# Kernel optimization log

Measured on AMD Instinct MI355X. Metric: run time of the kernel, lower is better.

## Reference

```python
import jax, jax.numpy as jnp
import numpy as np

TOPK = 13
NUM_CLASSES = 80
ALPHA = 1.0
BETA = 6.0
EPS = 1e-09
BS, NA, M = 8, 33600, 64
IMG = 1280.0


def setup_inputs() -> dict:
    key = jax.random.key(0)
    k = jax.random.split(key, 8)
    pd_scores = jax.random.uniform(k[0], (BS, NA, NUM_CLASSES), jnp.float32)
    pd_xy = jax.random.uniform(k[1], (BS, NA, 2), jnp.float32) * IMG
    pd_r = jax.random.uniform(k[2], (BS, NA, 1), jnp.float32) * 63.0 + 1.0
    pd_circles = jnp.concatenate([pd_xy, pd_r], axis=-1)
    anc_points = jax.random.uniform(k[3], (NA, 2), jnp.float32) * IMG
    gt_labels = jax.random.randint(k[4], (BS, M, 1), 0, NUM_CLASSES)
    gt_xy = jax.random.uniform(k[5], (BS, M, 2), jnp.float32) * IMG
    gt_r = jax.random.uniform(k[6], (BS, M, 1), jnp.float32) * 120.0 + 8.0
    gt_circles = jnp.concatenate([gt_xy, gt_r], axis=-1)
    mask_gt = (jax.random.uniform(k[7], (BS, M, 1)) > 0.2).astype(jnp.float32)
    return {"pd_scores": pd_scores, "pd_circles": pd_circles, "anc_points": anc_points,
            "gt_labels": gt_labels, "gt_circles": gt_circles, "mask_gt": mask_gt}


def _circle_iou(gt_circles, pd_circles):
    # gt_circles: (bs, M, 3); pd_circles: (bs, NA, 3) -> iou (bs, M, NA)
    c0 = gt_circles[:, :, None, :2]          # (bs, M, 1, 2)
    r0 = gt_circles[:, :, None, 2]           # (bs, M, 1)
    c1 = pd_circles[:, None, :, :2]          # (bs, 1, NA, 2)
    r1 = pd_circles[:, None, :, 2]           # (bs, 1, NA)
    d = jnp.sqrt(jnp.sum((c0 - c1) ** 2, axis=-1) + 1e-12)  # (bs, M, NA)
    # lens (partial-overlap) area, numerically safe
    d1 = (r0 ** 2 - r1 ** 2 + d ** 2) / (2.0 * d)
    d2 = d - d1
    a0 = r0 ** 2 * jnp.arccos(jnp.clip(d1 / jnp.maximum(r0, EPS), -1.0, 1.0)) \
         - d1 * jnp.sqrt(jnp.clip(r0 ** 2 - d1 ** 2, 0.0, None))
    a1 = r1 ** 2 * jnp.arccos(jnp.clip(d2 / jnp.maximum(r1, EPS), -1.0, 1.0)) \
         - d2 * jnp.sqrt(jnp.clip(r1 ** 2 - d2 ** 2, 0.0, None))
    lens = a0 + a1
    contained = jnp.pi * jnp.minimum(r0, r1) ** 2
    inter = jnp.where(d >= r0 + r1, 0.0, jnp.where(d <= jnp.abs(r0 - r1), contained, lens))
    area0 = jnp.pi * r0 ** 2
    area1 = jnp.pi * r1 ** 2
    union = area0 + area1 - inter
    return jnp.where(union > 0, inter / union, 0.0)


def _assigner(pd_scores, pd_circles, anc_points, gt_labels, gt_circles, mask_gt):
    bs, na, nc = pd_scores.shape
    m = gt_circles.shape[1]
    mask_gt_f = mask_gt[..., 0]  # (bs, m)

    # select_candidates_in_gts: anchor point inside gt circle
    d_anc = jnp.sqrt(jnp.sum((anc_points[None, None, :, :] - gt_circles[:, :, None, :2]) ** 2, axis=-1))
    mask_in_gts = (d_anc < gt_circles[:, :, None, 2]).astype(pd_scores.dtype)  # (bs, m, na)
    mask_valid = mask_in_gts * mask_gt_f[:, :, None]

    # get_box_metrics: gather class scores at gt label, circle IoU, align metric
    gl = jnp.clip(gt_labels[..., 0], 0, nc - 1)  # (bs, m) int
    ps_t = jnp.transpose(pd_scores, (0, 2, 1))   # (bs, nc, na)
    bbox_scores = jnp.take_along_axis(ps_t, jnp.broadcast_to(gl[:, :, None], (bs, m, na)), axis=1)
    bbox_scores = bbox_scores * mask_valid
    overlaps = _circle_iou(gt_circles, pd_circles) * mask_valid  # (bs, m, na)
    align_metric = (bbox_scores ** ALPHA) * (overlaps ** BETA)

    # select_topk_candidates
    topk_metrics, topk_idxs = jax.lax.top_k(align_metric, TOPK)   # (bs, m, topk)
    topk_mask = jnp.broadcast_to(mask_gt_f[:, :, None] > 0, topk_idxs.shape)
    topk_idxs = jnp.where(topk_mask, topk_idxs, 0)
    counts = jnp.zeros((bs, m, na), pd_scores.dtype).at[
        jnp.arange(bs)[:, None, None], jnp.arange(m)[None, :, None], topk_idxs].add(1.0)
    mask_topk = jnp.where(counts > 1, 0.0, counts)
    mask_pos = mask_topk * mask_in_gts * mask_gt_f[:, :, None]

    # select_highest_overlaps: resolve anchors assigned to multiple gts
    fg = jnp.sum(mask_pos, axis=1)                       # (bs, na)
    multi = (fg[:, None, :] > 1)                          # (bs, 1->m, na)
    max_idx = jnp.argmax(overlaps, axis=1)                # (bs, na)
    is_max = jax.nn.one_hot(max_idx, m, axis=1, dtype=mask_pos.dtype)  # (bs, m, na)
    mask_pos = jnp.where(multi, is_max, mask_pos)
    fg_mask = jnp.sum(mask_pos, axis=1)                   # (bs, na)
    target_gt_idx = jnp.argmax(mask_pos, axis=1)          # (bs, na)

    # get_targets
    bidx = jnp.arange(bs)[:, None]
    target_labels = jnp.clip(gt_labels[..., 0][bidx, target_gt_idx], 0, None)   # (bs, na)
    target_circles = gt_circles[bidx, target_gt_idx]                             # (bs, na, 3)
    target_scores = jax.nn.one_hot(target_labels, nc, dtype=pd_scores.dtype)
    target_scores = jnp.where(fg_mask[..., None] > 0, target_scores, 0.0)

    # normalize scores by aligned metric
    am = align_metric * mask_pos
    pos_align = jnp.max(am, axis=-1, keepdims=True)                # (bs, m, 1)
    pos_overlaps = jnp.max(overlaps * mask_pos, axis=-1, keepdims=True)
    norm = jnp.max(am * pos_overlaps / (pos_align + EPS), axis=1)[..., None]  # (bs, na, 1)
    target_scores = target_scores * norm
    return target_labels, target_circles, target_scores, fg_mask > 0, target_gt_idx


def reference(pd_scores, pd_circles, anc_points, gt_labels, gt_circles, mask_gt):
    return _assigner(pd_scores, pd_circles, anc_points, gt_labels, gt_circles, mask_gt)
```

## Files before the change

### kernel.cpp

```cpp
#include <hip/hip_runtime.h>
#include <math.h>

#define B   8
#define NA  33600
#define M   64
#define NC  80
#define KK  13
#define EPSF 1e-9f
#define PIF 3.14159265358979323846f

#define NPOS 1536
#define NBM  (B * M)
#define SPB  (M * KK)


__device__ __forceinline__ float circle_iou(float gx, float gy, float gr,
                                            float px, float py, float pr) {
    float dx = gx - px, dy = gy - py;
    float d  = sqrtf(dx * dx + dy * dy + 1e-12f);
    float r0sq = gr * gr, r1sq = pr * pr;
    float d1 = (r0sq - r1sq + d * d) / (2.0f * d);
    float d2 = d - d1;
    float t0 = fminf(fmaxf(d1 / fmaxf(gr, EPSF), -1.0f), 1.0f);
    float t1 = fminf(fmaxf(d2 / fmaxf(pr, EPSF), -1.0f), 1.0f);
    float a0 = r0sq * acosf(t0) - d1 * sqrtf(fmaxf(r0sq - d1 * d1, 0.0f));
    float a1 = r1sq * acosf(t1) - d2 * sqrtf(fmaxf(r1sq - d2 * d2, 0.0f));
    float lens = a0 + a1;
    float rmin = fminf(gr, pr);
    float contained = PIF * rmin * rmin;
    float inter = (d >= gr + pr) ? 0.0f
                : ((d <= fabsf(gr - pr)) ? contained : lens);
    float uni = PIF * r0sq + PIF * r1sq - inter;
    return (uni > 0.0f) ? inter / uni : 0.0f;
}


__global__ __launch_bounds__(1024)
void k_discover(const float* __restrict__ pd_scores, const float* __restrict__ pd_circles,
                const float* __restrict__ anc, const int* __restrict__ gt_labels,
                const float* __restrict__ gt_circles, const float* __restrict__ mask_gt,
                int* __restrict__ wlist, int* __restrict__ assigned,
                float* __restrict__ am_val) {
    int bm = blockIdx.x;
    int b  = bm / M;
    int tid = threadIdx.x;

    const int SL = (B * NA) / NBM;
    int s0 = bm * SL;
    if (tid < SL) { assigned[s0 + tid] = -1; am_val[s0 + tid] = 0.0f; }

    __shared__ int   s_pcnt;
    __shared__ int   s_pa[NPOS];
    __shared__ float s_pv[NPOS];
    __shared__ int   s_win[KK];

    float gmask = mask_gt[bm];
    if (!(gmask > 0.0f)) {
        if (tid < KK) wlist[bm * KK + tid] = -1;
        return;
    }

    float gx = gt_circles[bm * 3 + 0];
    float gy = gt_circles[bm * 3 + 1];
    float gr = gt_circles[bm * 3 + 2];
    int gl = gt_labels[bm];
    gl = gl < 0 ? 0 : (gl > NC - 1 ? NC - 1 : gl);

    if (tid == 0) s_pcnt = 0;
    __syncthreads();

    const float2* pdc2 = reinterpret_cast<const float2*>(pd_circles + (size_t)b * NA * 3);
    for (int q = tid; q < NA / 2; q += 1024) {
        float4 ap = reinterpret_cast<const float4*>(anc)[q];
        float2 p0 = pdc2[3 * q + 0];
        float2 p1 = pdc2[3 * q + 1];
        float2 p2 = pdc2[3 * q + 2];
        {
            float dx = ap.x - gx, dy = ap.y - gy;
            if (sqrtf(dx * dx + dy * dy) < gr) {
                float px = p0.x, py = p0.y, pr = p1.x;
                float cdx = gx - px, cdy = gy - py;
                float dc = sqrtf(cdx * cdx + cdy * cdy + 1e-12f);
                if (dc < gr + pr) {
                    float ov = circle_iou(gx, gy, gr, px, py, pr);
                    if (ov > 0.0f) {
                        float sc = pd_scores[((size_t)b * NA + 2 * q) * NC + gl];
                        float o2 = ov * ov;
                        float met = sc * (o2 * o2 * o2);
                        if (met > 0.0f) {
                            int p = atomicAdd(&s_pcnt, 1);
                            if (p < NPOS) { s_pa[p] = 2 * q; s_pv[p] = met; }
                        }
                    }
                }
            }
        }
        {
            float dx = ap.z - gx, dy = ap.w - gy;
            if (sqrtf(dx * dx + dy * dy) < gr) {
                float px = p1.y, py = p2.x, pr = p2.y;
                float cdx = gx - px, cdy = gy - py;
                float dc = sqrtf(cdx * cdx + cdy * cdy + 1e-12f);
                if (dc < gr + pr) {
                    float ov = circle_iou(gx, gy, gr, px, py, pr);
                    if (ov > 0.0f) {
                        float sc = pd_scores[((size_t)b * NA + 2 * q + 1) * NC + gl];
                        float o2 = ov * ov;
                        float met = sc * (o2 * o2 * o2);
                        if (met > 0.0f) {
                            int p = atomicAdd(&s_pcnt, 1);
                            if (p < NPOS) { s_pa[p] = 2 * q + 1; s_pv[p] = met; }
                        }
                    }
                }
            }
        }
    }
    __syncthreads();
    int pcnt = s_pcnt; if (pcnt > NPOS) pcnt = NPOS;

    if (tid >= 64) return;

    for (int k = 0; k < KK; k++) {
        float bv = 0.0f; int ba = 0x7fffffff; int bp = -1;
        for (int i = tid; i < pcnt; i += 64) {
            float v = s_pv[i];
            if (v > 0.0f) {
                int a = s_pa[i];
                if (v > bv || (v == bv && a < ba)) { bv = v; ba = a; bp = i; }
            }
        }
        for (int off = 32; off > 0; off >>= 1) {
            float v2 = __shfl_xor(bv, off);
            int   a2 = __shfl_xor(ba, off);
            int   p2 = __shfl_xor(bp, off);
            if (v2 > bv || (v2 == bv && a2 < ba)) { bv = v2; ba = a2; bp = p2; }
        }
        if (tid == 0) {
            if (bp >= 0) { s_win[k] = ba; s_pv[bp] = -1.0f; }
            else s_win[k] = -2;
        }
    }

    int defmask = 0;
    for (int k = 0; k < KK; k++) if (s_win[k] == -2) defmask |= (1 << k);
    if (defmask) {
        int base = 0;
        while (defmask && base < NA) {
            int idx = base + tid;
            bool freez = (idx < NA);
            for (int i = 0; i < pcnt; i++)
                freez = freez && (s_pa[i] != idx);
            unsigned long long msk = __ballot(freez);
            while (msk && defmask) {
                int bit = __ffsll((long long)msk) - 1; msk &= msk - 1;
                int k2  = __ffs(defmask) - 1;          defmask &= defmask - 1;
                if (tid == 0) s_win[k2] = base + bit;
            }
            base += 64;
        }
        while (defmask) {
            int k2 = __ffs(defmask) - 1; defmask &= defmask - 1;
            if (tid == 0) s_win[k2] = -1;
        }
    }

    if (tid < KK) {
        int a = s_win[tid];
        int outv = -1;
        if (a >= 0) {
            float ax = anc[2 * a], ay = anc[2 * a + 1];
            float dx = ax - gx, dy = ay - gy;
            if (sqrtf(dx * dx + dy * dy) < gr) outv = a;
        }
        wlist[bm * KK + tid] = outv;
    }
}


__global__ __launch_bounds__(1024)
void k_resolve(const float* __restrict__ pd_scores, const float* __restrict__ pd_circles,
               const float* __restrict__ anc, const int* __restrict__ gt_labels,
               const float* __restrict__ gt_circles, const float* __restrict__ mask_gt,
               const int* __restrict__ wlist,
               int* __restrict__ assigned, float* __restrict__ am_val,
               int* __restrict__ pos_align_i, int* __restrict__ pos_ov_i) {
    int b = blockIdx.x;
    int tid = threadIdx.x;

    __shared__ unsigned int s_cnt[NA / 4 + 1];
    __shared__ float s_gx[M], s_gy[M], s_gr[M];
    __shared__ int   s_gl[M], s_act[M];
    __shared__ int   s_posa[M], s_poso[M];
    __shared__ int   s_multi[512];
    __shared__ int   s_nm;

    if (tid < M) {
        int gi = b * M + tid;
        s_act[tid] = mask_gt[gi] > 0.0f;
        s_gx[tid] = gt_circles[gi * 3 + 0];
        s_gy[tid] = gt_circles[gi * 3 + 1];
        s_gr[tid] = gt_circles[gi * 3 + 2];
        int l = gt_labels[gi];
        s_gl[tid] = l < 0 ? 0 : (l > NC - 1 ? NC - 1 : l);
        s_posa[tid] = 0; s_poso[tid] = 0;
    }
    if (tid == 0) s_nm = 0;
    for (int w = tid; w < NA / 4 + 1; w += 1024) s_cnt[w] = 0;
    __syncthreads();

    int a = -1, m = -1; unsigned int prev = 0;
    if (tid < SPB) {
        a = wlist[b * SPB + tid];
        m = tid / KK;
        if (a >= 0) {
            unsigned int sh = 8u * (a & 3);
            unsigned int old = atomicAdd(&s_cnt[a >> 2], 1u << sh);
            prev = (old >> sh) & 0xFFu;
        }
    }
    __syncthreads();

    bool single = false;
    if (a >= 0) {
        unsigned int c = (s_cnt[a >> 2] >> (8u * (a & 3))) & 0xFFu;
        if (c == 1u) single = true;
        else if (prev == 0u) { int i2 = atomicAdd(&s_nm, 1); s_multi[i2] = a; }
    }
    if (single) {
        int i = b * NA + a;
        float gx = s_gx[m], gy = s_gy[m], gr = s_gr[m];
        float px = pd_circles[(size_t)i * 3 + 0];
        float py = pd_circles[(size_t)i * 3 + 1];
        float pr = pd_circles[(size_t)i * 3 + 2];
        float cdx = gx - px, cdy = gy - py;
        float dc = sqrtf(cdx * cdx + cdy * cdy + 1e-12f);
        float ov = (dc >= gr + pr) ? 0.0f : circle_iou(gx, gy, gr, px, py, pr);
        float met = 0.0f;
        if (ov > 0.0f) {
            float sc = pd_scores[(size_t)i * NC + s_gl[m]];
            float o2 = ov * ov;
            met = sc * (o2 * o2 * o2);
        }
        assigned[i] = m;
        am_val[i]   = met;
        atomicMax(&s_posa[m], __float_as_int(met));
        atomicMax(&s_poso[m], __float_as_int(ov));
    }
    __syncthreads();

    int lane = tid & 63, w = tid >> 6;
    int nm = s_nm;
    for (int r = w; r < nm; r += 16) {
        int am_ = s_multi[r];
        int i = b * NA + am_;
        float ax = anc[2 * am_], ay = anc[2 * am_ + 1];
        float px = pd_circles[(size_t)i * 3 + 0];
        float py = pd_circles[(size_t)i * 3 + 1];
        float pr = pd_circles[(size_t)i * 3 + 2];
        float ov = 0.0f;
        if (s_act[lane]) {
            float gx = s_gx[lane], gy = s_gy[lane], gr = s_gr[lane];
            float dx = ax - gx, dy = ay - gy;
            if (sqrtf(dx * dx + dy * dy) < gr) {
                float cdx = gx - px, cdy = gy - py;
                float dc = sqrtf(cdx * cdx + cdy * cdy + 1e-12f);
                ov = (dc >= gr + pr) ? 0.0f : circle_iou(gx, gy, gr, px, py, pr);
            }
        }
        float bv = ov; int bmx = lane;
        for (int off = 32; off > 0; off >>= 1) {
            float v2 = __shfl_xor(bv, off);
            int   m2 = __shfl_xor(bmx, off);
            if (v2 > bv || (v2 == bv && m2 < bmx)) { bv = v2; bmx = m2; }
        }
        if (lane == 0) {
            float met = 0.0f;
            if (bv > 0.0f) {
                float sc = pd_scores[(size_t)i * NC + s_gl[bmx]];
                float o2 = bv * bv;
                met = sc * (o2 * o2 * o2);
            }
            assigned[i] = bmx;
            am_val[i]   = met;
            atomicMax(&s_posa[bmx], __float_as_int(met));
            atomicMax(&s_poso[bmx], __float_as_int(bv));
        }
    }
    __syncthreads();

    if (tid < M) {
        pos_align_i[b * M + tid] = s_posa[tid];
        pos_ov_i[b * M + tid]    = s_poso[tid];
    }
}


__global__ void k_out(const int* __restrict__ assigned, const float* __restrict__ am_val,
                      const int* __restrict__ pos_align_i, const int* __restrict__ pos_ov_i,
                      const int* __restrict__ gt_labels, const float* __restrict__ gt_circles,
                      float* __restrict__ out_labels, float* __restrict__ out_circ,
                      float* __restrict__ out_scores, float* __restrict__ out_fg,
                      float* __restrict__ out_gtidx) {
    const int QPR = NC / 4;
    int q = blockIdx.x * blockDim.x + threadIdx.x;
    if (q >= B * NA * QPR) return;
    int row = q / QPR;
    int c0  = (q - row * QPR) * 4;
    int b   = row / NA;

    int g = assigned[row];
    int gidx = 0; float fg = 0.0f; float norm = 0.0f;
    if (g >= 0) {
        gidx = g; fg = 1.0f;
        float pa = __int_as_float(pos_align_i[b * M + g]);
        float po = __int_as_float(pos_ov_i[b * M + g]);
        norm = am_val[row] * po / (pa + EPSF);
    }
    int rawl = gt_labels[b * M + gidx];
    int lbl = rawl < 0 ? 0 : rawl;

    float4 v = make_float4(0.f, 0.f, 0.f, 0.f);
    if (g >= 0) {
        int off = lbl - c0;
        if (off >= 0 && off < 4) ((float*)&v)[off] = norm;
    }
    reinterpret_cast<float4*>(out_scores)[q] = v;

    if (c0 == 0) {
        out_labels[row] = (float)lbl;
        out_circ[(size_t)row * 3 + 0] = gt_circles[(b * M + gidx) * 3 + 0];
        out_circ[(size_t)row * 3 + 1] = gt_circles[(b * M + gidx) * 3 + 1];
        out_circ[(size_t)row * 3 + 2] = gt_circles[(b * M + gidx) * 3 + 2];
        out_fg[row]    = fg;
        out_gtidx[row] = (float)gidx;
    }
}


extern "C" void kernel_launch(void* const* d_in, const int* in_sizes, int n_in,
                              void* d_out, int out_size, void* d_ws, size_t ws_size,
                              hipStream_t stream) {
    const float* pd_scores  = (const float*)d_in[0];
    const float* pd_circles = (const float*)d_in[1];
    const float* anc        = (const float*)d_in[2];
    const int*   gt_labels  = (const int*)  d_in[3];
    const float* gt_circles = (const float*)d_in[4];
    const float* mask_gt    = (const float*)d_in[5];

    char* w = (char*)d_ws;
    int*   wlist       = (int*)w;   w += (size_t)NBM * KK * sizeof(int);
    int*   assigned    = (int*)w;   w += (size_t)B * NA * sizeof(int);
    float* am_val      = (float*)w; w += (size_t)B * NA * sizeof(float);
    int*   pos_align_i = (int*)w;   w += (size_t)B * M * sizeof(int);
    int*   pos_ov_i    = (int*)w;   w += (size_t)B * M * sizeof(int);

    float* out        = (float*)d_out;
    float* out_labels = out;
    float* out_circ   = out_labels + (size_t)B * NA;
    float* out_scores = out_circ + (size_t)B * NA * 3;
    float* out_fg     = out_scores + (size_t)B * NA * NC;
    float* out_gtidx  = out_fg + (size_t)B * NA;

    k_discover<<<NBM, 1024, 0, stream>>>(pd_scores, pd_circles, anc, gt_labels,
                                         gt_circles, mask_gt,
                                         wlist, assigned, am_val);

    k_resolve<<<B, 1024, 0, stream>>>(pd_scores, pd_circles, anc, gt_labels,
                                      gt_circles, mask_gt, wlist,
                                      assigned, am_val, pos_align_i, pos_ov_i);

    int nq = B * NA * (NC / 4);
    k_out<<<(nq + 255) / 256, 256, 0, stream>>>(assigned, am_val,
                                                pos_align_i, pos_ov_i,
                                                gt_labels, gt_circles,
                                                out_labels, out_circ, out_scores,
                                                out_fg, out_gtidx);
}
```

Before: 83.19 us.

## Invert discovery loop to anchor-major chunks and move top-k into resolve kernel

The per-(batch,gt) discovery kernel, which streamed all 33600 anchors once for every gt, is replaced by an anchor-chunk kernel. Each thread loads one anchor's prediction once and tests it against all 64 gts held in shared memory, writing compacted (anchor,gt,metric) candidates to per-chunk regions. The resolve kernel then gathers these candidates into a shared pool, runs per-gt top-k selection with one wave per gt, and reuses the stored metric instead of recomputing it. This removes 64x redundant anchor reads, but top-k now runs in only 8 blocks, and the fixed candidate capacities (96 per chunk, 96 per gt) can silently drop candidates.

```diff
diff --git a/kernel.cpp b/kernel.cpp
--- a/kernel.cpp
+++ b/kernel.cpp
@@ -9,9 +9,12 @@
 #define EPSF 1e-9f
 #define PIF 3.14159265358979323846f
 
-#define NPOS 1536
-#define NBM  (B * M)
-#define SPB  (M * KK)
+#define CHK   256
+#define NCHK  132
+#define BCAP  96
+#define REG   (1 + 2 * BCAP)
+#define FCAP  4096
+#define GCAP  96
 
 
 __device__ __forceinline__ float circle_iou(float gx, float gy, float gr,
@@ -35,165 +38,98 @@
 }
 
 
+__global__ __launch_bounds__(CHK)
+void k_build(const float* __restrict__ pd_scores, const float* __restrict__ pd_circles,
+             const float* __restrict__ anc, const int* __restrict__ gt_labels,
+             const float* __restrict__ gt_circles, const float* __restrict__ mask_gt,
+             int* __restrict__ breg, int* __restrict__ assigned,
+             float* __restrict__ am_val) {
+    int chunk = blockIdx.x;
+    int b     = blockIdx.y;
+    int tid   = threadIdx.x;
+
+    __shared__ float s_gx[M], s_gy[M], s_gr[M];
+    __shared__ int   s_gl[M], s_act[M];
+    __shared__ int   s_cnt;
+    __shared__ int   s_pk[BCAP];
+    __shared__ int   s_mv[BCAP];
+
+    if (tid < M) {
+        int gi = b * M + tid;
+        s_act[tid] = mask_gt[gi] > 0.0f;
+        s_gx[tid] = gt_circles[gi * 3 + 0];
+        s_gy[tid] = gt_circles[gi * 3 + 1];
+        s_gr[tid] = gt_circles[gi * 3 + 2];
+        int l = gt_labels[gi];
+        s_gl[tid] = l < 0 ? 0 : (l > NC - 1 ? NC - 1 : l);
+    }
+    if (tid == 0) s_cnt = 0;
+    __syncthreads();
+
+    int a = chunk * CHK + tid;
+    if (a < NA) {
+        int i = b * NA + a;
+        assigned[i] = -1;
+        am_val[i]   = 0.0f;
+        float2 ap = reinterpret_cast<const float2*>(anc)[a];
+        float px = pd_circles[(size_t)i * 3 + 0];
+        float py = pd_circles[(size_t)i * 3 + 1];
+        float pr = pd_circles[(size_t)i * 3 + 2];
+
+        for (int m = 0; m < M; m++) {
+            if (!s_act[m]) continue;
+            float gx = s_gx[m], gy = s_gy[m], gr = s_gr[m];
+            float dxa = ap.x - gx, dya = ap.y - gy;
+            if (!(sqrtf(dxa * dxa + dya * dya) < gr)) continue;
+            float cdx = gx - px, cdy = gy - py;
+            float dc = sqrtf(cdx * cdx + cdy * cdy + 1e-12f);
+            if (dc >= gr + pr) continue;
+            float ov = circle_iou(gx, gy, gr, px, py, pr);
+            if (!(ov > 0.0f)) continue;
+            float sc = pd_scores[(size_t)i * NC + s_gl[m]];
+            float o2 = ov * ov;
+            float met = sc * (o2 * o2 * o2);
+            if (met > 0.0f) {
+                int p = atomicAdd(&s_cnt, 1);
+                if (p < BCAP) { s_pk[p] = (a << 6) | m; s_mv[p] = __float_as_int(met); }
+            }
+        }
+    }
+    __syncthreads();
+
+    int cnt = s_cnt; if (cnt > BCAP) cnt = BCAP;
+    int rbase = (b * NCHK + chunk) * REG;
+    if (tid == 0) breg[rbase] = cnt;
+    if (tid < cnt) {
+        breg[rbase + 1 + tid]        = s_pk[tid];
+        breg[rbase + 1 + BCAP + tid] = s_mv[tid];
+    }
+}
+
+
 __global__ __launch_bounds__(1024)
-void k_discover(const float* __restrict__ pd_scores, const float* __restrict__ pd_circles,
-                const float* __restrict__ anc, const int* __restrict__ gt_labels,
-                const float* __restrict__ gt_circles, const float* __restrict__ mask_gt,
-                int* __restrict__ wlist, int* __restrict__ assigned,
-                float* __restrict__ am_val) {
-    int bm = blockIdx.x;
-    int b  = bm / M;
-    int tid = threadIdx.x;
-
-    const int SL = (B * NA) / NBM;
-    int s0 = bm * SL;
-    if (tid < SL) { assigned[s0 + tid] = -1; am_val[s0 + tid] = 0.0f; }
-
-    __shared__ int   s_pcnt;
-    __shared__ int   s_pa[NPOS];
-    __shared__ float s_pv[NPOS];
-    __shared__ int   s_win[KK];
-
-    float gmask = mask_gt[bm];
-    if (!(gmask > 0.0f)) {
-        if (tid < KK) wlist[bm * KK + tid] = -1;
-        return;
-    }
-
-    float gx = gt_circles[bm * 3 + 0];
-    float gy = gt_circles[bm * 3 + 1];
-    float gr = gt_circles[bm * 3 + 2];
-    int gl = gt_labels[bm];
-    gl = gl < 0 ? 0 : (gl > NC - 1 ? NC - 1 : gl);
-
-    if (tid == 0) s_pcnt = 0;
-    __syncthreads();
-
-    const float2* pdc2 = reinterpret_cast<const float2*>(pd_circles + (size_t)b * NA * 3);
-    for (int q = tid; q < NA / 2; q += 1024) {
-        float4 ap = reinterpret_cast<const float4*>(anc)[q];
-        float2 p0 = pdc2[3 * q + 0];
-        float2 p1 = pdc2[3 * q + 1];
-        float2 p2 = pdc2[3 * q + 2];
-        {
-            float dx = ap.x - gx, dy = ap.y - gy;
-            if (sqrtf(dx * dx + dy * dy) < gr) {
-                float px = p0.x, py = p0.y, pr = p1.x;
-                float cdx = gx - px, cdy = gy - py;
-                float dc = sqrtf(cdx * cdx + cdy * cdy + 1e-12f);
-                if (dc < gr + pr) {
-                    float ov = circle_iou(gx, gy, gr, px, py, pr);
-                    if (ov > 0.0f) {
-                        float sc = pd_scores[((size_t)b * NA + 2 * q) * NC + gl];
-                        float o2 = ov * ov;
-                        float met = sc * (o2 * o2 * o2);
-                        if (met > 0.0f) {
-                            int p = atomicAdd(&s_pcnt, 1);
-                            if (p < NPOS) { s_pa[p] = 2 * q; s_pv[p] = met; }
-                        }
-                    }
-                }
-            }
-        }
-        {
-            float dx = ap.z - gx, dy = ap.w - gy;
-            if (sqrtf(dx * dx + dy * dy) < gr) {
-                float px = p1.y, py = p2.x, pr = p2.y;
-                float cdx = gx - px, cdy = gy - py;
-                float dc = sqrtf(cdx * cdx + cdy * cdy + 1e-12f);
-                if (dc < gr + pr) {
-                    float ov = circle_iou(gx, gy, gr, px, py, pr);
-                    if (ov > 0.0f) {
-                        float sc = pd_scores[((size_t)b * NA + 2 * q + 1) * NC + gl];
-                        float o2 = ov * ov;
-                        float met = sc * (o2 * o2 * o2);
-                        if (met > 0.0f) {
-                            int p = atomicAdd(&s_pcnt, 1);
-                            if (p < NPOS) { s_pa[p] = 2 * q + 1; s_pv[p] = met; }
-                        }
-                    }
-                }
-            }
-        }
-    }
-    __syncthreads();
-    int pcnt = s_pcnt; if (pcnt > NPOS) pcnt = NPOS;
-
-    if (tid >= 64) return;
-
-    for (int k = 0; k < KK; k++) {
-        float bv = 0.0f; int ba = 0x7fffffff; int bp = -1;
-        for (int i = tid; i < pcnt; i += 64) {
-            float v = s_pv[i];
-            if (v > 0.0f) {
-                int a = s_pa[i];
-                if (v > bv || (v == bv && a < ba)) { bv = v; ba = a; bp = i; }
-            }
-        }
-        for (int off = 32; off > 0; off >>= 1) {
-            float v2 = __shfl_xor(bv, off);
-            int   a2 = __shfl_xor(ba, off);
-            int   p2 = __shfl_xor(bp, off);
-            if (v2 > bv || (v2 == bv && a2 < ba)) { bv = v2; ba = a2; bp = p2; }
-        }
-        if (tid == 0) {
-            if (bp >= 0) { s_win[k] = ba; s_pv[bp] = -1.0f; }
-            else s_win[k] = -2;
-        }
-    }
-
-    int defmask = 0;
-    for (int k = 0; k < KK; k++) if (s_win[k] == -2) defmask |= (1 << k);
-    if (defmask) {
-        int base = 0;
-        while (defmask && base < NA) {
-            int idx = base + tid;
-            bool freez = (idx < NA);
-            for (int i = 0; i < pcnt; i++)
-                freez = freez && (s_pa[i] != idx);
-            unsigned long long msk = __ballot(freez);
-            while (msk && defmask) {
-                int bit = __ffsll((long long)msk) - 1; msk &= msk - 1;
-                int k2  = __ffs(defmask) - 1;          defmask &= defmask - 1;
-                if (tid == 0) s_win[k2] = base + bit;
-            }
-            base += 64;
-        }
-        while (defmask) {
-            int k2 = __ffs(defmask) - 1; defmask &= defmask - 1;
-            if (tid == 0) s_win[k2] = -1;
-        }
-    }
-
-    if (tid < KK) {
-        int a = s_win[tid];
-        int outv = -1;
-        if (a >= 0) {
-            float ax = anc[2 * a], ay = anc[2 * a + 1];
-            float dx = ax - gx, dy = ay - gy;
-            if (sqrtf(dx * dx + dy * dy) < gr) outv = a;
-        }
-        wlist[bm * KK + tid] = outv;
-    }
-}
-
-
-__global__ __launch_bounds__(1024)
-void k_resolve(const float* __restrict__ pd_scores, const float* __restrict__ pd_circles,
-               const float* __restrict__ anc, const int* __restrict__ gt_labels,
-               const float* __restrict__ gt_circles, const float* __restrict__ mask_gt,
-               const int* __restrict__ wlist,
-               int* __restrict__ assigned, float* __restrict__ am_val,
-               int* __restrict__ pos_align_i, int* __restrict__ pos_ov_i) {
-    int b = blockIdx.x;
-    int tid = threadIdx.x;
-
-    __shared__ unsigned int s_cnt[NA / 4 + 1];
+void k_sel_resolve(const float* __restrict__ pd_scores, const float* __restrict__ pd_circles,
+                   const float* __restrict__ anc, const int* __restrict__ gt_labels,
+                   const float* __restrict__ gt_circles, const float* __restrict__ mask_gt,
+                   const int* __restrict__ breg,
+                   int* __restrict__ assigned, float* __restrict__ am_val,
+                   int* __restrict__ pos_align_i, int* __restrict__ pos_ov_i) {
+    int b    = blockIdx.x;
+    int tid  = threadIdx.x;
+    int lane = tid & 63;
+    int w    = tid >> 6;
+
+    __shared__ unsigned s_pool[8448];
+    __shared__ int   s_gla[16][GCAP];
+    __shared__ float s_glv[16][GCAP];
+    __shared__ int   s_glcnt[16];
+    __shared__ int   s_win[M * KK];
+    __shared__ float s_wmet[M * KK];
     __shared__ float s_gx[M], s_gy[M], s_gr[M];
     __shared__ int   s_gl[M], s_act[M];
     __shared__ int   s_posa[M], s_poso[M];
-    __shared__ int   s_multi[512];
-    __shared__ int   s_nm;
+    __shared__ int   s_multi[M * KK];
+    __shared__ int   s_nm, s_fcnt;
 
     if (tid < M) {
         int gi = b * M + tid;
@@ -205,51 +141,143 @@
         s_gl[tid] = l < 0 ? 0 : (l > NC - 1 ? NC - 1 : l);
         s_posa[tid] = 0; s_poso[tid] = 0;
     }
-    if (tid == 0) s_nm = 0;
-    for (int w = tid; w < NA / 4 + 1; w += 1024) s_cnt[w] = 0;
-    __syncthreads();
-
-    int a = -1, m = -1; unsigned int prev = 0;
-    if (tid < SPB) {
-        a = wlist[b * SPB + tid];
-        m = tid / KK;
+    if (tid == 0) { s_nm = 0; s_fcnt = 0; }
+    __syncthreads();
+
+    for (int r = w; r < NCHK; r += 16) {
+        int rbase = (b * NCHK + r) * REG;
+        int cnt = breg[rbase];
+        int ofs = 0;
+        if (lane == 0) ofs = atomicAdd(&s_fcnt, cnt);
+        ofs = __shfl(ofs, 0);
+        for (int j = lane; j < cnt; j += 64) {
+            int dst = ofs + j;
+            if (dst < FCAP) {
+                s_pool[dst]        = (unsigned)breg[rbase + 1 + j];
+                s_pool[4096 + dst] = (unsigned)breg[rbase + 1 + BCAP + j];
+            }
+        }
+    }
+    __syncthreads();
+    int fcnt = s_fcnt; if (fcnt > FCAP) fcnt = FCAP;
+
+    for (int q = 0; q < 4; q++) {
+        int m = w * 4 + q;
+        bool active = s_act[m] != 0;
+        if (lane == 0) s_glcnt[w] = 0;
+        __syncthreads();
+        if (active) {
+            for (int i = lane; i < fcnt; i += 64) {
+                unsigned pk = s_pool[i];
+                if ((pk & 63u) == (unsigned)m) {
+                    float v = __uint_as_float(s_pool[4096 + i]);
+                    int p = atomicAdd(&s_glcnt[w], 1);
+                    if (p < GCAP) { s_gla[w][p] = (int)(pk >> 6); s_glv[w][p] = v; }
+                }
+            }
+        }
+        __syncthreads();
+        int cnt = 0;
+        if (active) { cnt = s_glcnt[w]; if (cnt > GCAP) cnt = GCAP; }
+
+        for (int k = 0; k < KK; k++) {
+            if (!active) break;
+            float bv = 0.0f; int ba = 0x7fffffff; int bp = -1;
+            for (int i = lane; i < cnt; i += 64) {
+                float v = s_glv[w][i];
+                if (v > 0.0f) {
+                    int a = s_gla[w][i];
+                    if (v > bv || (v == bv && a < ba)) { bv = v; ba = a; bp = i; }
+                }
+            }
+            for (int off = 32; off > 0; off >>= 1) {
+                float v2 = __shfl_xor(bv, off);
+                int   a2 = __shfl_xor(ba, off);
+                int   p2 = __shfl_xor(bp, off);
+                if (v2 > bv || (v2 == bv && a2 < ba)) { bv = v2; ba = a2; bp = p2; }
+            }
+            if (lane == 0) {
+                int slot = m * KK + k;
+                if (bp >= 0) { s_win[slot] = ba; s_wmet[slot] = bv; s_glv[w][bp] = -1.0f; }
+                else         { s_win[slot] = -2; s_wmet[slot] = 0.0f; }
+            }
+        }
+
+        if (active) {
+            int defmask = 0;
+            for (int k = 0; k < KK; k++) if (s_win[m * KK + k] == -2) defmask |= (1 << k);
+            if (defmask) {
+                int base = 0;
+                while (defmask && base < NA) {
+                    int idx = base + lane;
+                    bool freez = (idx < NA);
+                    for (int i = 0; i < cnt; i++)
+                        freez = freez && (s_gla[w][i] != idx);
+                    unsigned long long msk = __ballot(freez);
+                    while (msk && defmask) {
+                        int bit = __ffsll((long long)msk) - 1; msk &= msk - 1;
+                        int k2  = __ffs(defmask) - 1;          defmask &= defmask - 1;
+                        if (lane == 0) { s_win[m * KK + k2] = base + bit; s_wmet[m * KK + k2] = 0.0f; }
+                    }
+                    base += 64;
+                }
+                while (defmask) {
+                    int k2 = __ffs(defmask) - 1; defmask &= defmask - 1;
+                    if (lane == 0) s_win[m * KK + k2] = -1;
+                }
+            }
+            if (lane < KK) {
+                int slot = m * KK + lane;
+                int a = s_win[slot];
+                if (a >= 0) {
+                    float ax = anc[2 * a], ay = anc[2 * a + 1];
+                    float dx = ax - s_gx[m], dy = ay - s_gy[m];
+                    if (!(sqrtf(dx * dx + dy * dy) < s_gr[m])) s_win[slot] = -1;
+                } else s_win[slot] = -1;
+            }
+        } else {
+            if (lane < KK) s_win[m * KK + lane] = -1;
+        }
+    }
+    __syncthreads();
+
+    for (int i = tid; i < NA / 4 + 1; i += 1024) s_pool[i] = 0;
+    __syncthreads();
+    int mya = -1, mym = -1; unsigned prev = 0;
+    if (tid < M * KK) {
+        int a = s_win[tid];
+        mym = tid / KK;
         if (a >= 0) {
-            unsigned int sh = 8u * (a & 3);
-            unsigned int old = atomicAdd(&s_cnt[a >> 2], 1u << sh);
+            mya = a;
+            unsigned sh = 8u * (a & 3);
+            unsigned old = atomicAdd(&s_pool[a >> 2], 1u << sh);
             prev = (old >> sh) & 0xFFu;
         }
     }
     __syncthreads();
 
-    bool single = false;
-    if (a >= 0) {
-        unsigned int c = (s_cnt[a >> 2] >> (8u * (a & 3))) & 0xFFu;
-        if (c == 1u) single = true;
-        else if (prev == 0u) { int i2 = atomicAdd(&s_nm, 1); s_multi[i2] = a; }
-    }
-    if (single) {
-        int i = b * NA + a;
-        float gx = s_gx[m], gy = s_gy[m], gr = s_gr[m];
-        float px = pd_circles[(size_t)i * 3 + 0];
-        float py = pd_circles[(size_t)i * 3 + 1];
-        float pr = pd_circles[(size_t)i * 3 + 2];
-        float cdx = gx - px, cdy = gy - py;
-        float dc = sqrtf(cdx * cdx + cdy * cdy + 1e-12f);
-        float ov = (dc >= gr + pr) ? 0.0f : circle_iou(gx, gy, gr, px, py, pr);
-        float met = 0.0f;
-        if (ov > 0.0f) {
-            float sc = pd_scores[(size_t)i * NC + s_gl[m]];
-            float o2 = ov * ov;
-            met = sc * (o2 * o2 * o2);
-        }
-        assigned[i] = m;
-        am_val[i]   = met;
-        atomicMax(&s_posa[m], __float_as_int(met));
-        atomicMax(&s_poso[m], __float_as_int(ov));
-    }
-    __syncthreads();
-
-    int lane = tid & 63, w = tid >> 6;
+    if (mya >= 0) {
+        unsigned c = (s_pool[mya >> 2] >> (8u * (mya & 3))) & 0xFFu;
+        if (c == 1u) {
+            int i = b * NA + mya;
+            float met = s_wmet[tid];
+            float gx = s_gx[mym], gy = s_gy[mym], gr = s_gr[mym];
+            float px = pd_circles[(size_t)i * 3 + 0];
+            float py = pd_circles[(size_t)i * 3 + 1];
+            float pr = pd_circles[(size_t)i * 3 + 2];
+            float cdx = gx - px, cdy = gy - py;
+            float dc = sqrtf(cdx * cdx + cdy * cdy + 1e-12f);
+            float ov = (dc >= gr + pr) ? 0.0f : circle_iou(gx, gy, gr, px, py, pr);
+            assigned[i] = mym;
+            am_val[i]   = met;
+            atomicMax(&s_posa[mym], __float_as_int(met));
+            atomicMax(&s_poso[mym], __float_as_int(ov));
+        } else if (prev == 0u) {
+            int p = atomicAdd(&s_nm, 1); s_multi[p] = mya;
+        }
+    }
+    __syncthreads();
+
     int nm = s_nm;
     for (int r = w; r < nm; r += 16) {
         int am_ = s_multi[r];
@@ -349,7 +377,7 @@
     const float* mask_gt    = (const float*)d_in[5];
 
     char* w = (char*)d_ws;
-    int*   wlist       = (int*)w;   w += (size_t)NBM * KK * sizeof(int);
+    int*   breg        = (int*)w;   w += (size_t)B * NCHK * REG * sizeof(int);
     int*   assigned    = (int*)w;   w += (size_t)B * NA * sizeof(int);
     float* am_val      = (float*)w; w += (size_t)B * NA * sizeof(float);
     int*   pos_align_i = (int*)w;   w += (size_t)B * M * sizeof(int);
@@ -362,13 +390,13 @@
     float* out_fg     = out_scores + (size_t)B * NA * NC;
     float* out_gtidx  = out_fg + (size_t)B * NA;
 
-    k_discover<<<NBM, 1024, 0, stream>>>(pd_scores, pd_circles, anc, gt_labels,
-                                         gt_circles, mask_gt,
-                                         wlist, assigned, am_val);
-
-    k_resolve<<<B, 1024, 0, stream>>>(pd_scores, pd_circles, anc, gt_labels,
-                                      gt_circles, mask_gt, wlist,
-                                      assigned, am_val, pos_align_i, pos_ov_i);
+    dim3 gb(NCHK, B);
+    k_build<<<gb, CHK, 0, stream>>>(pd_scores, pd_circles, anc, gt_labels,
+                                    gt_circles, mask_gt, breg, assigned, am_val);
+
+    k_sel_resolve<<<B, 1024, 0, stream>>>(pd_scores, pd_circles, anc, gt_labels,
+                                          gt_circles, mask_gt, breg,
+                                          assigned, am_val, pos_align_i, pos_ov_i);
 
     int nq = B * NA * (NC / 4);
     k_out<<<(nq + 255) / 256, 256, 0, stream>>>(assigned, am_val,
```

Measured after the change: 146.9 us. +76.5%, slower.

## Process two GTs per discover block and simplify resolve with cached metrics

Applied to the files above, without the earlier changes.

The discover kernel now handles two ground-truth objects per block (256 blocks instead of 512), so each anchor and prediction load is reused for both, and it records the winning metric and overlap per slot. The resolve kernel is split across 32 smaller blocks. It reuses the cached metric and overlap for anchors claimed by a single GT, recomputes only the multi-claimed ones serially per thread, and does atomicMax directly in global memory. This cuts redundant global reads and the large shared-memory counter array, at the cost of more shared memory per discover block, an O(SPB) duplicate scan per resolve thread, and global atomics.

```diff
diff --git a/kernel.cpp b/kernel.cpp
--- a/kernel.cpp
+++ b/kernel.cpp
@@ -10,8 +10,8 @@
 #define PIF 3.14159265358979323846f
 
 #define NPOS 1536
-#define NBM  (B * M)
 #define SPB  (M * KK)
+#define NDIS 256
 
 
 __device__ __forceinline__ float circle_iou(float gx, float gy, float gr,
@@ -39,35 +39,59 @@
 void k_discover(const float* __restrict__ pd_scores, const float* __restrict__ pd_circles,
                 const float* __restrict__ anc, const int* __restrict__ gt_labels,
                 const float* __restrict__ gt_circles, const float* __restrict__ mask_gt,
-                int* __restrict__ wlist, int* __restrict__ assigned,
-                float* __restrict__ am_val) {
-    int bm = blockIdx.x;
-    int b  = bm / M;
+                int* __restrict__ wlist, float* __restrict__ wmet, float* __restrict__ wov,
+                int* __restrict__ assigned, float* __restrict__ am_val,
+                int* __restrict__ pos_align_i, int* __restrict__ pos_ov_i) {
+    int bid = blockIdx.x;
+    int b   = bid >> 5;
+    int j   = bid & 31;
+    int m0  = 2 * j;
     int tid = threadIdx.x;
 
-    const int SL = (B * NA) / NBM;
-    int s0 = bm * SL;
-    if (tid < SL) { assigned[s0 + tid] = -1; am_val[s0 + tid] = 0.0f; }
-
-    __shared__ int   s_pcnt;
-    __shared__ int   s_pa[NPOS];
-    __shared__ float s_pv[NPOS];
-    __shared__ int   s_win[KK];
-
-    float gmask = mask_gt[bm];
-    if (!(gmask > 0.0f)) {
-        if (tid < KK) wlist[bm * KK + tid] = -1;
+    const int SL = (B * NA) / NDIS;
+    for (int i = tid; i < SL; i += 1024) {
+        assigned[bid * SL + i] = -1;
+        am_val[bid * SL + i]   = 0.0f;
+    }
+    if (j == 0 && tid < M) { pos_align_i[b * M + tid] = 0; pos_ov_i[b * M + tid] = 0; }
+
+    __shared__ int   s_cnt[2];
+    __shared__ int   s_pa[2][NPOS];
+    __shared__ float s_pv[2][NPOS];
+    __shared__ float s_po[2][NPOS];
+    __shared__ int   s_win[2][KK];
+    __shared__ float s_selv[2][KK], s_selo[2][KK];
+
+    int bm0 = b * M + m0;
+    bool act0 = mask_gt[bm0]     > 0.0f;
+    bool act1 = mask_gt[bm0 + 1] > 0.0f;
+    if (!act0 && !act1) {
+        if (tid < KK) { wlist[bm0 * KK + tid] = -1; wlist[(bm0 + 1) * KK + tid] = -1; }
         return;
     }
-
-    float gx = gt_circles[bm * 3 + 0];
-    float gy = gt_circles[bm * 3 + 1];
-    float gr = gt_circles[bm * 3 + 2];
-    int gl = gt_labels[bm];
-    gl = gl < 0 ? 0 : (gl > NC - 1 ? NC - 1 : gl);
-
-    if (tid == 0) s_pcnt = 0;
+    float gx0 = gt_circles[bm0 * 3 + 0], gy0 = gt_circles[bm0 * 3 + 1], gr0 = gt_circles[bm0 * 3 + 2];
+    float gx1 = gt_circles[(bm0 + 1) * 3 + 0], gy1 = gt_circles[(bm0 + 1) * 3 + 1], gr1 = gt_circles[(bm0 + 1) * 3 + 2];
+    int gl0 = gt_labels[bm0];     gl0 = gl0 < 0 ? 0 : (gl0 > NC - 1 ? NC - 1 : gl0);
+    int gl1 = gt_labels[bm0 + 1]; gl1 = gl1 < 0 ? 0 : (gl1 > NC - 1 ? NC - 1 : gl1);
+
+    if (tid < 2) s_cnt[tid] = 0;
     __syncthreads();
+
+#define TRY(A_, AX_, AY_, PX_, PY_, PR_, G_, GX_, GY_, GR_, GL_) do {          \
+        float dx_ = (AX_) - (GX_), dy_ = (AY_) - (GY_);                        \
+        if (sqrtf(dx_ * dx_ + dy_ * dy_) < (GR_)) {                            \
+            float cdx_ = (GX_) - (PX_), cdy_ = (GY_) - (PY_);                  \
+            float dc_ = sqrtf(cdx_ * cdx_ + cdy_ * cdy_ + 1e-12f);             \
+            if (dc_ < (GR_) + (PR_)) {                                         \
+                float ov_ = circle_iou((GX_), (GY_), (GR_), (PX_), (PY_), (PR_)); \
+                if (ov_ > 0.0f) {                                              \
+                    float sc_ = pd_scores[((size_t)b * NA + (A_)) * NC + (GL_)]; \
+                    float o2_ = ov_ * ov_;                                     \
+                    float met_ = sc_ * (o2_ * o2_ * o2_);                      \
+                    if (met_ > 0.0f) {                                         \
+                        int p_ = atomicAdd(&s_cnt[G_], 1);                     \
+                        if (p_ < NPOS) { s_pa[G_][p_] = (A_); s_pv[G_][p_] = met_; s_po[G_][p_] = ov_; } \
+                    } } } } } while (0)
 
     const float2* pdc2 = reinterpret_cast<const float2*>(pd_circles + (size_t)b * NA * 3);
     for (int q = tid; q < NA / 2; q += 1024) {
@@ -75,58 +99,31 @@
         float2 p0 = pdc2[3 * q + 0];
         float2 p1 = pdc2[3 * q + 1];
         float2 p2 = pdc2[3 * q + 2];
-        {
-            float dx = ap.x - gx, dy = ap.y - gy;
-            if (sqrtf(dx * dx + dy * dy) < gr) {
-                float px = p0.x, py = p0.y, pr = p1.x;
-                float cdx = gx - px, cdy = gy - py;
-                float dc = sqrtf(cdx * cdx + cdy * cdy + 1e-12f);
-                if (dc < gr + pr) {
-                    float ov = circle_iou(gx, gy, gr, px, py, pr);
-                    if (ov > 0.0f) {
-                        float sc = pd_scores[((size_t)b * NA + 2 * q) * NC + gl];
-                        float o2 = ov * ov;
-                        float met = sc * (o2 * o2 * o2);
-                        if (met > 0.0f) {
-                            int p = atomicAdd(&s_pcnt, 1);
-                            if (p < NPOS) { s_pa[p] = 2 * q; s_pv[p] = met; }
-                        }
-                    }
-                }
-            }
-        }
-        {
-            float dx = ap.z - gx, dy = ap.w - gy;
-            if (sqrtf(dx * dx + dy * dy) < gr) {
-                float px = p1.y, py = p2.x, pr = p2.y;
-                float cdx = gx - px, cdy = gy - py;
-                float dc = sqrtf(cdx * cdx + cdy * cdy + 1e-12f);
-                if (dc < gr + pr) {
-                    float ov = circle_iou(gx, gy, gr, px, py, pr);
-                    if (ov > 0.0f) {
-                        float sc = pd_scores[((size_t)b * NA + 2 * q + 1) * NC + gl];
-                        float o2 = ov * ov;
-                        float met = sc * (o2 * o2 * o2);
-                        if (met > 0.0f) {
-                            int p = atomicAdd(&s_pcnt, 1);
-                            if (p < NPOS) { s_pa[p] = 2 * q + 1; s_pv[p] = met; }
-                        }
-                    }
-                }
-            }
-        }
-    }
+        int a0 = 2 * q, a1 = 2 * q + 1;
+        if (act0) TRY(a0, ap.x, ap.y, p0.x, p0.y, p1.x, 0, gx0, gy0, gr0, gl0);
+        if (act1) TRY(a0, ap.x, ap.y, p0.x, p0.y, p1.x, 1, gx1, gy1, gr1, gl1);
+        if (act0) TRY(a1, ap.z, ap.w, p1.y, p2.x, p2.y, 0, gx0, gy0, gr0, gl0);
+        if (act1) TRY(a1, ap.z, ap.w, p1.y, p2.x, p2.y, 1, gx1, gy1, gr1, gl1);
+    }
+#undef TRY
     __syncthreads();
-    int pcnt = s_pcnt; if (pcnt > NPOS) pcnt = NPOS;
-
-    if (tid >= 64) return;
+
+    int w = tid >> 6;
+    if (w >= 2) return;
+    int lane = tid & 63;
+    int m  = m0 + w;
+    int bm = b * M + m;
+    bool act = w ? act1 : act0;
+    if (!act) { if (lane < KK) wlist[bm * KK + lane] = -1; return; }
+    float gx = w ? gx1 : gx0, gy = w ? gy1 : gy0, gr = w ? gr1 : gr0;
+    int pcnt = s_cnt[w]; if (pcnt > NPOS) pcnt = NPOS;
 
     for (int k = 0; k < KK; k++) {
         float bv = 0.0f; int ba = 0x7fffffff; int bp = -1;
-        for (int i = tid; i < pcnt; i += 64) {
-            float v = s_pv[i];
+        for (int i = lane; i < pcnt; i += 64) {
+            float v = s_pv[w][i];
             if (v > 0.0f) {
-                int a = s_pa[i];
+                int a = s_pa[w][i];
                 if (v > bv || (v == bv && a < ba)) { bv = v; ba = a; bp = i; }
             }
         }
@@ -136,64 +133,71 @@
             int   p2 = __shfl_xor(bp, off);
             if (v2 > bv || (v2 == bv && a2 < ba)) { bv = v2; ba = a2; bp = p2; }
         }
-        if (tid == 0) {
-            if (bp >= 0) { s_win[k] = ba; s_pv[bp] = -1.0f; }
-            else s_win[k] = -2;
+        if (lane == 0) {
+            if (bp >= 0) {
+                s_win[w][k] = ba; s_selv[w][k] = bv; s_selo[w][k] = s_po[w][bp];
+                s_pv[w][bp] = -1.0f;
+            } else { s_win[w][k] = -2; s_selv[w][k] = 0.0f; s_selo[w][k] = 0.0f; }
         }
     }
 
     int defmask = 0;
-    for (int k = 0; k < KK; k++) if (s_win[k] == -2) defmask |= (1 << k);
+    for (int k = 0; k < KK; k++) if (s_win[w][k] == -2) defmask |= (1 << k);
     if (defmask) {
         int base = 0;
         while (defmask && base < NA) {
-            int idx = base + tid;
+            int idx = base + lane;
             bool freez = (idx < NA);
             for (int i = 0; i < pcnt; i++)
-                freez = freez && (s_pa[i] != idx);
+                freez = freez && (s_pa[w][i] != idx);
             unsigned long long msk = __ballot(freez);
             while (msk && defmask) {
                 int bit = __ffsll((long long)msk) - 1; msk &= msk - 1;
                 int k2  = __ffs(defmask) - 1;          defmask &= defmask - 1;
-                if (tid == 0) s_win[k2] = base + bit;
+                if (lane == 0) s_win[w][k2] = base + bit;
             }
             base += 64;
         }
         while (defmask) {
             int k2 = __ffs(defmask) - 1; defmask &= defmask - 1;
-            if (tid == 0) s_win[k2] = -1;
-        }
-    }
-
-    if (tid < KK) {
-        int a = s_win[tid];
-        int outv = -1;
+            if (lane == 0) s_win[w][k2] = -1;
+        }
+    }
+
+    if (lane < KK) {
+        int a = s_win[w][lane];
+        int outv = -1; float om = 0.0f, oo = 0.0f;
         if (a >= 0) {
             float ax = anc[2 * a], ay = anc[2 * a + 1];
             float dx = ax - gx, dy = ay - gy;
-            if (sqrtf(dx * dx + dy * dy) < gr) outv = a;
-        }
-        wlist[bm * KK + tid] = outv;
-    }
-}
-
-
-__global__ __launch_bounds__(1024)
+            if (sqrtf(dx * dx + dy * dy) < gr) {
+                outv = a; om = s_selv[w][lane]; oo = s_selo[w][lane];
+            }
+        }
+        wlist[bm * KK + lane] = outv;
+        wmet[bm * KK + lane]  = om;
+        wov[bm * KK + lane]   = oo;
+    }
+}
+
+
+__global__ __launch_bounds__(256)
 void k_resolve(const float* __restrict__ pd_scores, const float* __restrict__ pd_circles,
                const float* __restrict__ anc, const int* __restrict__ gt_labels,
                const float* __restrict__ gt_circles, const float* __restrict__ mask_gt,
-               const int* __restrict__ wlist,
+               const int* __restrict__ wlist, const float* __restrict__ wmet,
+               const float* __restrict__ wov,
                int* __restrict__ assigned, float* __restrict__ am_val,
                int* __restrict__ pos_align_i, int* __restrict__ pos_ov_i) {
-    int b = blockIdx.x;
-    int tid = threadIdx.x;
-
-    __shared__ unsigned int s_cnt[NA / 4 + 1];
+    int bid  = blockIdx.x;
+    int b    = bid >> 2;
+    int part = bid & 3;
+    int tid  = threadIdx.x;
+
+    __shared__ int   s_wl[SPB];
+    __shared__ float s_wm[SPB], s_wo[SPB];
     __shared__ float s_gx[M], s_gy[M], s_gr[M];
     __shared__ int   s_gl[M], s_act[M];
-    __shared__ int   s_posa[M], s_poso[M];
-    __shared__ int   s_multi[512];
-    __shared__ int   s_nm;
 
     if (tid < M) {
         int gi = b * M + tid;
@@ -203,95 +207,60 @@
         s_gr[tid] = gt_circles[gi * 3 + 2];
         int l = gt_labels[gi];
         s_gl[tid] = l < 0 ? 0 : (l > NC - 1 ? NC - 1 : l);
-        s_posa[tid] = 0; s_poso[tid] = 0;
-    }
-    if (tid == 0) s_nm = 0;
-    for (int w = tid; w < NA / 4 + 1; w += 1024) s_cnt[w] = 0;
+    }
+    for (int i = tid; i < SPB; i += 256) {
+        s_wl[i] = wlist[b * SPB + i];
+        s_wm[i] = wmet[b * SPB + i];
+        s_wo[i] = wov[b * SPB + i];
+    }
     __syncthreads();
 
-    int a = -1, m = -1; unsigned int prev = 0;
-    if (tid < SPB) {
-        a = wlist[b * SPB + tid];
-        m = tid / KK;
-        if (a >= 0) {
-            unsigned int sh = 8u * (a & 3);
-            unsigned int old = atomicAdd(&s_cnt[a >> 2], 1u << sh);
-            prev = (old >> sh) & 0xFFu;
-        }
-    }
-    __syncthreads();
-
-    bool single = false;
-    if (a >= 0) {
-        unsigned int c = (s_cnt[a >> 2] >> (8u * (a & 3))) & 0xFFu;
-        if (c == 1u) single = true;
-        else if (prev == 0u) { int i2 = atomicAdd(&s_nm, 1); s_multi[i2] = a; }
-    }
-    if (single) {
-        int i = b * NA + a;
-        float gx = s_gx[m], gy = s_gy[m], gr = s_gr[m];
+    int slot = part * (SPB / 4) + tid;
+    if (tid >= SPB / 4) return;
+    int a = s_wl[slot];
+    if (a < 0) return;
+
+    int cnt = 0, minslot = SPB;
+    for (int i2 = 0; i2 < SPB; i2++)
+        if (s_wl[i2] == a) { cnt++; if (i2 < minslot) minslot = i2; }
+    if (minslot != slot) return;
+
+    int i = b * NA + a;
+    if (cnt == 1) {
+        int m = slot / KK;
+        assigned[i] = m;
+        am_val[i]   = s_wm[slot];
+        atomicMax(&pos_align_i[b * M + m], __float_as_int(s_wm[slot]));
+        atomicMax(&pos_ov_i[b * M + m],    __float_as_int(s_wo[slot]));
+    } else {
+        float ax = anc[2 * a], ay = anc[2 * a + 1];
         float px = pd_circles[(size_t)i * 3 + 0];
         float py = pd_circles[(size_t)i * 3 + 1];
         float pr = pd_circles[(size_t)i * 3 + 2];
-        float cdx = gx - px, cdy = gy - py;
-        float dc = sqrtf(cdx * cdx + cdy * cdy + 1e-12f);
-        float ov = (dc >= gr + pr) ? 0.0f : circle_iou(gx, gy, gr, px, py, pr);
+        float best = -1.0f; int g = 0;
+        for (int mm = 0; mm < M; mm++) {
+            float ovv = 0.0f;
+            if (s_act[mm]) {
+                float gx = s_gx[mm], gy = s_gy[mm], gr = s_gr[mm];
+                float dx = ax - gx, dy = ay - gy;
+                if (sqrtf(dx * dx + dy * dy) < gr) {
+                    float cdx = gx - px, cdy = gy - py;
+                    float dc = sqrtf(cdx * cdx + cdy * cdy + 1e-12f);
+                    ovv = (dc >= gr + pr) ? 0.0f : circle_iou(gx, gy, gr, px, py, pr);
+                }
+            }
+            if (ovv > best) { best = ovv; g = mm; }
+        }
         float met = 0.0f;
-        if (ov > 0.0f) {
-            float sc = pd_scores[(size_t)i * NC + s_gl[m]];
-            float o2 = ov * ov;
+        if (best > 0.0f) {
+            float sc = pd_scores[(size_t)i * NC + s_gl[g]];
+            float o2 = best * best;
             met = sc * (o2 * o2 * o2);
         }
-        assigned[i] = m;
+        assigned[i] = g;
         am_val[i]   = met;
-        atomicMax(&s_posa[m], __float_as_int(met));
-        atomicMax(&s_poso[m], __float_as_int(ov));
-    }
-    __syncthreads();
-
-    int lane = tid & 63, w = tid >> 6;
-    int nm = s_nm;
-    for (int r = w; r < nm; r += 16) {
-        int am_ = s_multi[r];
-        int i = b * NA + am_;
-        float ax = anc[2 * am_], ay = anc[2 * am_ + 1];
-        float px = pd_circles[(size_t)i * 3 + 0];
-        float py = pd_circles[(size_t)i * 3 + 1];
-        float pr = pd_circles[(size_t)i * 3 + 2];
-        float ov = 0.0f;
-        if (s_act[lane]) {
-            float gx = s_gx[lane], gy = s_gy[lane], gr = s_gr[lane];
-            float dx = ax - gx, dy = ay - gy;
-            if (sqrtf(dx * dx + dy * dy) < gr) {
-                float cdx = gx - px, cdy = gy - py;
-                float dc = sqrtf(cdx * cdx + cdy * cdy + 1e-12f);
-                ov = (dc >= gr + pr) ? 0.0f : circle_iou(gx, gy, gr, px, py, pr);
-            }
-        }
-        float bv = ov; int bmx = lane;
-        for (int off = 32; off > 0; off >>= 1) {
-            float v2 = __shfl_xor(bv, off);
-            int   m2 = __shfl_xor(bmx, off);
-            if (v2 > bv || (v2 == bv && m2 < bmx)) { bv = v2; bmx = m2; }
-        }
-        if (lane == 0) {
-            float met = 0.0f;
-            if (bv > 0.0f) {
-                float sc = pd_scores[(size_t)i * NC + s_gl[bmx]];
-                float o2 = bv * bv;
-                met = sc * (o2 * o2 * o2);
-            }
-            assigned[i] = bmx;
-            am_val[i]   = met;
-            atomicMax(&s_posa[bmx], __float_as_int(met));
-            atomicMax(&s_poso[bmx], __float_as_int(bv));
-        }
-    }
-    __syncthreads();
-
-    if (tid < M) {
-        pos_align_i[b * M + tid] = s_posa[tid];
-        pos_ov_i[b * M + tid]    = s_poso[tid];
+        atomicMax(&pos_align_i[b * M + g], __float_as_int(met));
+        atomicMax(&pos_ov_i[b * M + g],    __float_as_int(fmaxf(best, 0.0f)));
     }
 }
 
@@ -349,7 +318,9 @@
     const float* mask_gt    = (const float*)d_in[5];
 
     char* w = (char*)d_ws;
-    int*   wlist       = (int*)w;   w += (size_t)NBM * KK * sizeof(int);
+    int*   wlist       = (int*)w;   w += (size_t)B * SPB * sizeof(int);
+    float* wmetv       = (float*)w; w += (size_t)B * SPB * sizeof(float);
+    float* wovv        = (float*)w; w += (size_t)B * SPB * sizeof(float);
     int*   assigned    = (int*)w;   w += (size_t)B * NA * sizeof(int);
     float* am_val      = (float*)w; w += (size_t)B * NA * sizeof(float);
     int*   pos_align_i = (int*)w;   w += (size_t)B * M * sizeof(int);
@@ -362,12 +333,13 @@
     float* out_fg     = out_scores + (size_t)B * NA * NC;
     float* out_gtidx  = out_fg + (size_t)B * NA;
 
-    k_discover<<<NBM, 1024, 0, stream>>>(pd_scores, pd_circles, anc, gt_labels,
-                                         gt_circles, mask_gt,
-                                         wlist, assigned, am_val);
-
-    k_resolve<<<B, 1024, 0, stream>>>(pd_scores, pd_circles, anc, gt_labels,
-                                      gt_circles, mask_gt, wlist,
+    k_discover<<<NDIS, 1024, 0, stream>>>(pd_scores, pd_circles, anc, gt_labels,
+                                          gt_circles, mask_gt,
+                                          wlist, wmetv, wovv,
+                                          assigned, am_val, pos_align_i, pos_ov_i);
+
+    k_resolve<<<32, 256, 0, stream>>>(pd_scores, pd_circles, anc, gt_labels,
+                                      gt_circles, mask_gt, wlist, wmetv, wovv,
                                       assigned, am_val, pos_align_i, pos_ov_i);
 
     int nq = B * NA * (NC / 4);
```

After: 113.1 us. 35.9% more time.
